# Kernel tuning notes

Hardware: AMD Instinct MI355X
Metric: run time of the kernel (lower is better)

Reference implementation:

```python
import jax, jax.numpy as jnp
import numpy as np

B_, S_, N_, D_ = 2, 128, 16, 6
HMV, HS, HEADS = 8, 24, 8

# ---- G(3,0,1) geometric algebra tables (16-dim multivectors) ----
_BLADES = [(), (0,), (1,), (2,), (3,), (0, 1), (0, 2), (0, 3), (1, 2), (1, 3), (2, 3), (0, 1, 2), (0, 1, 3), (0, 2, 3), (1, 2, 3), (0, 1, 2, 3)]
_IDX = {b: i for i, b in enumerate(_BLADES)}
_METRIC = [0.0, 1.0, 1.0, 1.0]  # e0^2=0 (projective), e1..e3^2=1

def _blade_mul(a, b):
    arr = list(a) + list(b)
    sign = 1.0
    i = 0
    while i < len(arr) - 1:
        if arr[i] > arr[i + 1]:
            arr[i], arr[i + 1] = arr[i + 1], arr[i]
            sign = -sign
            i = max(i - 1, 0)
        elif arr[i] == arr[i + 1]:
            sign *= _METRIC[arr[i]]
            del arr[i + 1]
            del arr[i]
            i = 0
        else:
            i += 1
    return sign, tuple(arr)

def _perm_sign(seq):
    s = 1.0
    for i in range(len(seq)):
        for j in range(i + 1, len(seq)):
            if seq[i] > seq[j]:
                s = -s
    return s

_GP_np = np.zeros((16, 16, 16), dtype=np.float32)
_WEDGE_np = np.zeros((16, 16, 16), dtype=np.float32)
for _a in _BLADES:
    for _b in _BLADES:
        _s, _r = _blade_mul(_a, _b)
        if _s != 0.0:
            _GP_np[_IDX[_r], _IDX[_a], _IDX[_b]] += _s
        if not set(_a) & set(_b):
            _WEDGE_np[_IDX[tuple(sorted(_a + _b))], _IDX[_a], _IDX[_b]] += _perm_sign(list(_a) + list(_b))

_DUAL_np = np.zeros((16, 16), dtype=np.float32)
for _b in _BLADES:
    _c = tuple(sorted(set((0, 1, 2, 3)) - set(_b)))
    _DUAL_np[_IDX[_c], _IDX[_b]] = _perm_sign(list(_b) + list(_c))

# 9 Pin-equivariant linear basis maps: 5 grade projections + 4 e0-wedge maps
_BASIS_np = np.zeros((9, 16, 16), dtype=np.float32)
for _i, _b in enumerate(_BLADES):
    _BASIS_np[len(_b), _i, _i] = 1.0
    if 0 not in _b and len(_b) <= 3:
        _BASIS_np[5 + len(_b), _IDX[(0,) + _b], _i] = 1.0

GP = jnp.asarray(_GP_np)
WEDGE = jnp.asarray(_WEDGE_np)
DUAL = jnp.asarray(_DUAL_np)
BASIS = jnp.asarray(_BASIS_np)
# invariant inner product uses the 8 non-e0 components
INNER = jnp.asarray(np.array([1, 0, 1, 1, 1, 0, 0, 0, 1, 1, 1, 0, 0, 0, 1, 0], dtype=np.float32))


def equi_linear(x_mv, x_s, w_mv, w_s2mv, w_m2s, w_s2s, b_mv, b_s):
    # x_mv [..., in_ch, 16] -> [..., out_ch, 16]; scalar channels mix via mv comp 0
    y = jnp.einsum('oik,kpq,...iq->...op', w_mv, BASIS, x_mv)
    extra = 0.0
    if w_s2mv is not None:
        extra = extra + jnp.einsum('oi,...i->...o', w_s2mv, x_s)
    if b_mv is not None:
        extra = extra + b_mv
    if w_s2mv is not None or b_mv is not None:
        y = y.at[..., 0].add(extra)
    y_s = None
    if w_m2s is not None:
        y_s = jnp.einsum('oi,...i->...o', w_m2s, x_mv[..., 0])
        if w_s2s is not None:
            y_s = y_s + jnp.einsum('oi,...i->...o', w_s2s, x_s)
        if b_s is not None:
            y_s = y_s + b_s
    return y, y_s


def equi_norm(x_mv, x_s, eps=1e-2):
    sq = jnp.sum(x_mv * x_mv * INNER, axis=-1)  # [..., ch]
    x_mv = x_mv / jnp.sqrt(jnp.mean(sq, axis=-1, keepdims=True) + eps)[..., None]
    x_s = x_s / jnp.sqrt(jnp.mean(x_s * x_s, axis=-1, keepdims=True) + eps)
    return x_mv, x_s


def join(a, b):
    da = jnp.einsum('pq,...q->...p', DUAL, a)
    db = jnp.einsum('pq,...q->...p', DUAL, b)
    w = jnp.einsum('kij,...i,...j->...k', WEDGE, da, db)
    return jnp.einsum('qp,...q->...p', DUAL, w)  # undual = DUAL^T (signed permutation)


def _forward(x, p):
    B, S, N, D = x.shape
    T = S * N
    xf = x.reshape(B, T, D)
    pos, vel = xf[..., 0:3], xf[..., 3:6]
    mv = jnp.zeros((B, T, 16), xf.dtype)
    mv = mv.at[..., 0].set(1.0)           # embed_scalar(mass=1)
    mv = mv.at[..., 14].set(1.0)          # embed_point: homogeneous e123
    mv = mv.at[..., 13].set(-pos[..., 0])
    mv = mv.at[..., 12].set(pos[..., 1])
    mv = mv.at[..., 11].set(-pos[..., 2])
    mv = mv.at[..., 5:8].set(0.5 * vel)   # embed_translation versor bivector part
    mv = mv[:, :, None, :]                # [B,T,1,16]

    times = jnp.arange(T) // N
    mask = times[:, None] >= times[None, :]  # causal over time blocks

    h_mv, h_s = equi_linear(mv, None, p['w_in_mv'], None, p['w_in_m2s'], None, p['b_in_mv'], p['b_in_s'])

    # --- equivariant self-attention block ---
    n_mv, n_s = equi_norm(h_mv, h_s)
    q_mv, q_s = equi_linear(n_mv, n_s, p['w_qkv_mv'][0], p['w_qkv_s2mv'][0], p['w_qkv_m2s'][0], p['w_qkv_s2s'][0], None, None)
    k_mv, k_s = equi_linear(n_mv, n_s, p['w_qkv_mv'][1], p['w_qkv_s2mv'][1], p['w_qkv_m2s'][1], p['w_qkv_s2s'][1], None, None)
    v_mv, v_s = equi_linear(n_mv, n_s, p['w_qkv_mv'][2], p['w_qkv_s2mv'][2], p['w_qkv_m2s'][2], p['w_qkv_s2s'][2], None, None)
    H = HEADS
    rs = lambda m, s: (m.reshape(B, T, H, HMV // H, 16), s.reshape(B, T, H, HS // H))
    q_mv, q_s = rs(q_mv, q_s)
    k_mv, k_s = rs(k_mv, k_s)
    v_mv, v_s = rs(v_mv, v_s)
    scale = 1.0 / np.sqrt(8.0 * (HMV // H) + HS // H)
    scores = (jnp.einsum('bthcq,q,bshcq->bhts', q_mv, INNER, k_mv)
              + jnp.einsum('bthd,bshd->bhts', q_s, k_s)) * scale
    scores = jnp.where(mask[None, None], scores, -1e30)
    attn = jax.nn.softmax(scores, axis=-1)
    o_mv = jnp.einsum('bhts,bshcq->bthcq', attn, v_mv).reshape(B, T, HMV, 16)
    o_s = jnp.einsum('bhts,bshd->bthd', attn, v_s).reshape(B, T, HS)
    a_mv, a_s = equi_linear(o_mv, o_s, p['w_ao_mv'], p['w_ao_s2mv'], p['w_ao_m2s'], p['w_ao_s2s'], p['b_ao_mv'], p['b_ao_s'])
    h_mv = h_mv + a_mv
    h_s = h_s + a_s

    # --- geometric MLP block ---
    n_mv, n_s = equi_norm(h_mv, h_s)
    u_mv, u_s = equi_linear(n_mv, n_s, p['w_m1_mv'], p['w_m1_s2mv'], p['w_m1_m2s'], p['w_m1_s2s'], p['b_m1_mv'], p['b_m1_s'])
    gl, gr, jl, jr = jnp.split(u_mv, 4, axis=-2)  # 4 groups of HMV/2 channels
    gp = jnp.einsum('kij,btci,btcj->btck', GP, gl, gr)  # geometric product
    jn = join(jl, jr)                                   # dual-based join
    g_mv = jnp.concatenate([gp, jn], axis=-2)           # [B,T,HMV,16]
    g_mv = g_mv * jax.nn.gelu(g_mv[..., 0:1], approximate=False)  # scalar-gated GELU
    g_s = jax.nn.gelu(u_s, approximate=False)
    m_mv, m_s = equi_linear(g_mv, g_s, p['w_m2_mv'], p['w_m2_s2mv'], p['w_m2_m2s'], p['w_m2_s2s'], p['b_m2_mv'], p['b_m2_s'])
    h_mv = h_mv + m_mv
    h_s = h_s + m_s

    out_mv, _ = equi_linear(h_mv, h_s, p['w_out_mv'], p['w_out_s2mv'], None, None, p['b_out_mv'], None)
    o = out_mv[:, :, 0, :]
    d = o[..., 14:15]
    d = jnp.where(jnp.abs(d) > 1e-3, d, jnp.where(d >= 0, 1e-3, -1e-3))  # safe homogeneous divide
    pred_pos = jnp.stack([-o[..., 13], o[..., 12], -o[..., 11]], axis=-1) / d  # extract_point
    pred_vel = 2.0 * o[..., 5:8]                                              # extract_translation
    return jnp.concatenate([pred_pos, pred_vel], axis=-1).reshape(B, S, N, D)


def setup_inputs() -> dict:
    key = jax.random.key(0)
    ks = iter(jax.random.split(key, 40))
    def nrm(shape, fan):
        return jax.random.normal(next(ks), shape, jnp.float32) / np.sqrt(fan)
    inp = {}
    inp['x'] = jax.random.normal(next(ks), (B_, S_, N_, D_), jnp.float32)
    inp['w_in_mv'] = nrm((HMV, 1, 9), 3.0)
    inp['b_in_mv'] = jnp.zeros((HMV,), jnp.float32)
    inp['w_in_m2s'] = nrm((HS, 1), 1.0)
    inp['b_in_s'] = jnp.zeros((HS,), jnp.float32)
    inp['w_qkv_mv'] = nrm((3, HMV, HMV, 9), 3.0 * HMV)
    inp['w_qkv_s2mv'] = nrm((3, HMV, HS), HS)
    inp['w_qkv_m2s'] = nrm((3, HS, HMV), HMV)
    inp['w_qkv_s2s'] = nrm((3, HS, HS), HS)
    inp['w_ao_mv'] = nrm((HMV, HMV, 9), 3.0 * HMV)
    inp['w_ao_s2mv'] = nrm((HMV, HS), HS)
    inp['w_ao_m2s'] = nrm((HS, HMV), HMV)
    inp['w_ao_s2s'] = nrm((HS, HS), HS)
    inp['b_ao_mv'] = jnp.zeros((HMV,), jnp.float32)
    inp['b_ao_s'] = jnp.zeros((HS,), jnp.float32)
    inp['w_m1_mv'] = nrm((2 * HMV, HMV, 9), 3.0 * HMV)
    inp['w_m1_s2mv'] = nrm((2 * HMV, HS), HS)
    inp['w_m1_m2s'] = nrm((HS, HMV), HMV)
    inp['w_m1_s2s'] = nrm((HS, HS), HS)
    inp['b_m1_mv'] = jnp.zeros((2 * HMV,), jnp.float32)
    inp['b_m1_s'] = jnp.zeros((HS,), jnp.float32)
    inp['w_m2_mv'] = nrm((HMV, HMV, 9), 3.0 * HMV)
    inp['w_m2_s2mv'] = nrm((HMV, HS), HS)
    inp['w_m2_m2s'] = nrm((HS, HMV), HMV)
    inp['w_m2_s2s'] = nrm((HS, HS), HS)
    inp['b_m2_mv'] = jnp.zeros((HMV,), jnp.float32)
    inp['b_m2_s'] = jnp.zeros((HS,), jnp.float32)
    inp['w_out_mv'] = nrm((1, HMV, 9), 3.0 * HMV)
    inp['w_out_s2mv'] = nrm((1, HS), HS)
    inp['b_out_mv'] = jnp.zeros((1,), jnp.float32)
    return inp


def reference(x, w_in_mv, b_in_mv, w_in_m2s, b_in_s, w_qkv_mv, w_qkv_s2mv, w_qkv_m2s, w_qkv_s2s, w_ao_mv, w_ao_s2mv, w_ao_m2s, w_ao_s2s, b_ao_mv, b_ao_s, w_m1_mv, w_m1_s2mv, w_m1_m2s, w_m1_s2s, b_m1_mv, b_m1_s, w_m2_mv, w_m2_s2mv, w_m2_m2s, w_m2_s2s, b_m2_mv, b_m2_s, w_out_mv, w_out_s2mv, b_out_mv):
    p = dict(locals())
    xx = p.pop('x')
    return _forward(xx, p)
```

## Files before the change

### kernel.cpp

```cpp
#include <hip/hip_runtime.h>
#include <math.h>

#define T_    2048
#define BTOK  4096
#define NSLOT 80

namespace {
constexpr int GRADE[16] = {0,1,1,1,1,2,2,2,2,2,2,3,3,3,3,4};
constexpr int AUGK[16]  = {-1,5,-1,-1,-1,6,6,6,-1,-1,-1,7,7,7,-1,8};
constexpr int AUGS[16]  = { 0,0, 0, 0, 0,2,3,4, 0, 0, 0,8,9,10,0,14};
constexpr float FINNER[16] = {1.f,0.f,1.f,1.f,1.f,0.f,0.f,0.f,1.f,1.f,1.f,0.f,0.f,0.f,1.f,0.f};
}

typedef __attribute__((ext_vector_type(4))) _Float16 h4_t;
typedef __attribute__((ext_vector_type(4))) float    f4_t;

__device__ __forceinline__ unsigned pkh(float a, float b){
  return __builtin_bit_cast(unsigned, __builtin_amdgcn_cvt_pkrtz(a,b));
}
__device__ __forceinline__ f4_t mfma16(h4_t a, h4_t b, f4_t c){
  return __builtin_amdgcn_mfma_f32_16x16x16f16(a,b,c,0,0,0);
}

__device__ __forceinline__ float gelu_f(float v){
  return 0.5f*v*(1.f + erff(v*0.70710678118654752f));
}

__device__ __forceinline__ int rsign_d(int a, int b){
  int s=0; a>>=1; while(a){ s += __popc(a&b); a>>=1; } return (s&1) ? -1 : 1;
}

__global__ void __launch_bounds__(64) k_in(
    const float* __restrict__ x,
    const float* __restrict__ w_in_mv, const float* __restrict__ b_in_mv,
    const float* __restrict__ w_in_m2s, const float* __restrict__ b_in_s,
    const float* __restrict__ w_mv, const float* __restrict__ w_s2mv,
    const float* __restrict__ w_m2s, const float* __restrict__ w_s2s,
    float* __restrict__ h_mv, float* __restrict__ h_s,
    unsigned* __restrict__ qph, unsigned* __restrict__ kph, unsigned* __restrict__ vph)
{
  __shared__ float NS[2*152];
  int tid=threadIdx.x, tl=tid>>5, ln=tid&31;
  int o=ln&7, iq=ln>>3;
  int tt=blockIdx.x*2+tl;
  int b=tt>>11, t=tt&(T_-1);
  const float* xp = x+(size_t)tt*6;
  float mv[16];
  #pragma unroll
  for(int p=0;p<16;p++) mv[p]=0.f;
  mv[0]=1.f; mv[14]=1.f;
  mv[13]=-xp[0]; mv[12]=xp[1]; mv[11]=-xp[2];
  mv[5]=0.5f*xp[3]; mv[6]=0.5f*xp[4]; mv[7]=0.5f*xp[5];

  const float* wo=w_in_mv+o*9;
  float h[16]; float sq=0.f;
  #pragma unroll
  for(int p=0;p<16;p++){
    float v=wo[GRADE[p]]*mv[p];
    if(AUGK[p]>=0) v+=wo[AUGK[p]]*mv[AUGS[p]];
    if(p==0) v+=b_in_mv[o];
    h[p]=v; sq+=FINNER[p]*v*v;
  }
  sq+=__shfl_xor(sq,1); sq+=__shfl_xor(sq,2); sq+=__shfl_xor(sq,4);
  float dmv=rsqrtf(sq*0.125f+0.01f);
  float hs[3]; float ssq=0.f;
  #pragma unroll
  for(int jj=0;jj<3;jj++){ float v=w_in_m2s[o*3+jj]+b_in_s[o*3+jj]; hs[jj]=v; ssq+=v*v; }
  ssq+=__shfl_xor(ssq,1); ssq+=__shfl_xor(ssq,2); ssq+=__shfl_xor(ssq,4);
  float dss=rsqrtf(ssq*(1.f/24.f)+0.01f);

  float* ns=&NS[tl*152];
  if(iq==0){
    float4* hg=(float4*)(h_mv+(size_t)tt*128+o*16);
    hg[0]=make_float4(h[0],h[1],h[2],h[3]);
    hg[1]=make_float4(h[4],h[5],h[6],h[7]);
    hg[2]=make_float4(h[8],h[9],h[10],h[11]);
    hg[3]=make_float4(h[12],h[13],h[14],h[15]);
    #pragma unroll
    for(int jj=0;jj<3;jj++) h_s[(size_t)tt*24+o*3+jj]=hs[jj];
    #pragma unroll
    for(int p=0;p<16;p++) ns[o*16+p]=h[p]*dmv;
    #pragma unroll
    for(int jj=0;jj<3;jj++) ns[128+o*3+jj]=hs[jj]*dss;
  }
  __syncthreads();

  float yq[16],yk[16],yv[16];
  #pragma unroll
  for(int p=0;p<16;p++){ yq[p]=0.f; yk[p]=0.f; yv[p]=0.f; }
  float nx0p[2];
  const float* wq=w_mv+o*72;
  #pragma unroll
  for(int ii=0;ii<2;ii++){
    int i=iq*2+ii;
    float xi[16];
    const float4* xs4=(const float4*)&ns[i*16];
    #pragma unroll
    for(int r4=0;r4<4;r4++){ float4 v=xs4[r4]; xi[r4*4]=v.x; xi[r4*4+1]=v.y; xi[r4*4+2]=v.z; xi[r4*4+3]=v.w; }
    nx0p[ii]=xi[0];
    const float* aq=wq+i*9; const float* ak=aq+576; const float* av=aq+1152;
    #pragma unroll
    for(int p=0;p<16;p++){
      float bb=xi[p];
      yq[p]+=aq[GRADE[p]]*bb; yk[p]+=ak[GRADE[p]]*bb; yv[p]+=av[GRADE[p]]*bb;
      if(AUGK[p]>=0){
        float au=xi[AUGS[p]];
        yq[p]+=aq[AUGK[p]]*au; yk[p]+=ak[AUGK[p]]*au; yv[p]+=av[AUGK[p]]*au;
      }
    }
  }
  float sq3[3]={0,0,0}, sk3[3]={0,0,0}, sv3[3]={0,0,0};
  float eq=0.f,ek=0.f,ev=0.f;
  for(int j=iq*6;j<iq*6+6;j++){
    float s=ns[128+j];
    eq+=w_s2mv[o*24+j]*s; ek+=w_s2mv[192+o*24+j]*s; ev+=w_s2mv[384+o*24+j]*s;
    #pragma unroll
    for(int jj=0;jj<3;jj++){
      int d=o*3+jj;
      sq3[jj]+=w_s2s[d*24+j]*s;
      sk3[jj]+=w_s2s[576+d*24+j]*s;
      sv3[jj]+=w_s2s[1152+d*24+j]*s;
    }
  }
  #pragma unroll
  for(int ii=0;ii<2;ii++){
    int i=iq*2+ii;
    #pragma unroll
    for(int jj=0;jj<3;jj++){
      int d=o*3+jj;
      sq3[jj]+=w_m2s[d*8+i]*nx0p[ii];
      sk3[jj]+=w_m2s[192+d*8+i]*nx0p[ii];
      sv3[jj]+=w_m2s[384+d*8+i]*nx0p[ii];
    }
  }
  yq[0]+=eq; yk[0]+=ek; yv[0]+=ev;
  #pragma unroll
  for(int p=0;p<16;p++){
    yq[p]+=__shfl_xor(yq[p],8);  yq[p]+=__shfl_xor(yq[p],16);
    yk[p]+=__shfl_xor(yk[p],8);  yk[p]+=__shfl_xor(yk[p],16);
    yv[p]+=__shfl_xor(yv[p],8);  yv[p]+=__shfl_xor(yv[p],16);
  }
  #pragma unroll
  for(int jj=0;jj<3;jj++){
    sq3[jj]+=__shfl_xor(sq3[jj],8); sq3[jj]+=__shfl_xor(sq3[jj],16);
    sk3[jj]+=__shfl_xor(sk3[jj],8); sk3[jj]+=__shfl_xor(sk3[jj],16);
    sv3[jj]+=__shfl_xor(sv3[jj],8); sv3[jj]+=__shfl_xor(sv3[jj],16);
  }

  const float scale = 0.3015113445777636f;
  size_t rb=((size_t)(b*8+o)*T_+t);
  if(iq==0){
    uint4 qa,qb;
    qa.x=pkh(yq[0]*scale, yq[2]*scale);  qa.y=pkh(yq[3]*scale, yq[4]*scale);
    qa.z=pkh(yq[8]*scale, yq[9]*scale);  qa.w=pkh(yq[10]*scale, yq[14]*scale);
    qb.x=pkh(sq3[0]*scale, sq3[1]*scale); qb.y=pkh(sq3[2]*scale, 0.f); qb.z=0u; qb.w=0u;
    uint4* qr4=(uint4*)qph + rb*2; qr4[0]=qa; qr4[1]=qb;
  } else if(iq==1){
    uint4 ka,kb;
    ka.x=pkh(yk[0],yk[2]);  ka.y=pkh(yk[3],yk[4]);
    ka.z=pkh(yk[8],yk[9]);  ka.w=pkh(yk[10],yk[14]);
    kb.x=pkh(sk3[0],sk3[1]); kb.y=pkh(sk3[2],0.f); kb.z=0u; kb.w=0u;
    uint4* kr4=(uint4*)kph + rb*2; kr4[0]=ka; kr4[1]=kb;
  }
  {
    size_t vbase2 = (size_t)(b*8+o)*(T_/16)*256;
    size_t cidx   = (size_t)(t>>4);
    int    wp     = (t>>1)&7;
    size_t tb     = vbase2 + cidx*256;
    bool even = (tl==0);
    if(iq==2){
      #pragma unroll
      for(int c=0;c<10;c++){
        float other=__shfl_xor(yv[c],32);
        if(even) vph[tb + c*8 + wp]=pkh(yv[c],other);
      }
    } else if(iq==3){
      #pragma unroll
      for(int c=10;c<16;c++){
        float other=__shfl_xor(yv[c],32);
        if(even) vph[tb + c*8 + wp]=pkh(yv[c],other);
      }
      #pragma unroll
      for(int jj=0;jj<3;jj++){
        float other=__shfl_xor(sv3[jj],32);
        if(even) vph[tb + (16+jj)*8 + wp]=pkh(sv3[jj],other);
      }
      if(even) vph[tb + 19*8 + wp]=0x3C003C00u;
    }
    if(even){
      int c0=20+iq*3;
      #pragma unroll
      for(int cc=0;cc<3;cc++) vph[tb + (c0+cc)*8 + wp]=0u;
    }
  }
}

__global__ void __launch_bounds__(256) k_attn(
    const unsigned* __restrict__ qph, const unsigned* __restrict__ kph,
    const unsigned* __restrict__ vph,
    float* __restrict__ part)
{
  int tid=threadIdx.x;
  int wave=tid>>6, lane=tid&63;
  int col=lane&15, rowb=lane>>4;
  int j=blockIdx.x;
  int bh=j&15;
  int z=NSLOT-1-(j>>4);
  int a=0;
  while (4*(a+1)*(a+2) <= z) a++;
  int rem = z - 4*a*(a+1);
  int bqd = rem/(a+1);
  int sp  = rem - bqd*(a+1);
  int strip = 8*a + bqd;
  int c     = a+1;
  int nchunk = (strip+1)*4;
  int t0 = sp*nchunk/c, t1 = (sp+1)*nchunk/c;
  int chend = strip*4 + wave + 1;
  if (t1 < chend) chend = t1;

  int q0 = strip*64 + wave*16;
  const h4_t* qh4=(const h4_t*)qph;
  const h4_t* kh4=(const h4_t*)kph;
  const h4_t* vh4=(const h4_t*)vph;

  h4_t bq = qh4[((size_t)bh*T_ + q0 + col)*4 + rowb];

  f4_t acc0={0.f,0.f,0.f,0.f}, acc1={0.f,0.f,0.f,0.f};
  size_t vtile = (size_t)bh*(T_/16)*128;
  int voff0 = col*4 + rowb;
  int voff1 = 64 + col*4 + rowb;

  #pragma unroll 4
  for(int ch=t0; ch<chend; ++ch){
    h4_t ak = kh4[((size_t)bh*T_ + 16*ch + col)*4 + rowb];
    f4_t zz={0.f,0.f,0.f,0.f};
    f4_t st = mfma16(ak, bq, zz);
    float c0=fminf(__expf(st[0]),60000.f);
    float c1=fminf(__expf(st[1]),60000.f);
    float c2=fminf(__expf(st[2]),60000.f);
    float c3=fminf(__expf(st[3]),60000.f);
    h4_t bp = __builtin_bit_cast(h4_t, make_uint2(pkh(c0,c1), pkh(c2,c3)));
    h4_t av0 = vh4[vtile + (size_t)ch*128 + voff0];
    h4_t av1 = vh4[vtile + (size_t)ch*128 + voff1];
    acc0 = mfma16(av0, bp, acc0);
    acc1 = mfma16(av1, bp, acc1);
  }

  float* rec = part + (((size_t)bh*NSLOT + z)*64 + wave*16 + col)*20;
  ((float4*)rec)[rowb] = make_float4(acc0[0],acc0[1],acc0[2],acc0[3]);
  if(rowb==0) ((float4*)rec)[4] = make_float4(acc1[0],acc1[1],acc1[2],acc1[3]);
}

__global__ void __launch_bounds__(64) k_tail(
    const float* __restrict__ part,
    const float* __restrict__ w_ao_mv, const float* __restrict__ w_ao_s2mv,
    const float* __restrict__ w_ao_m2s, const float* __restrict__ w_ao_s2s,
    const float* __restrict__ b_ao_mv, const float* __restrict__ b_ao_s,
    const float* __restrict__ h_mv, const float* __restrict__ h_s,
    const float* __restrict__ w_m1_mv, const float* __restrict__ w_m1_s2mv,
    const float* __restrict__ w_m1_m2s, const float* __restrict__ w_m1_s2s,
    const float* __restrict__ b_m1_mv, const float* __restrict__ b_m1_s,
    const float* __restrict__ w_m2_mv, const float* __restrict__ w_m2_s2mv,
    const float* __restrict__ b_m2_mv,
    const float* __restrict__ w_out_mv,
    float* __restrict__ out)
{
  __shared__ int   GPI[256]; __shared__ float GPS[256];
  __shared__ int   JNI[256]; __shared__ float JNS[256];
  __shared__ float OS[2*152];
  __shared__ float NS[2*152];
  __shared__ float U[2*264];
  __shared__ float G[2*136];
  __shared__ float GSm[2*24];
  int tid=threadIdx.x, tl=tid>>5, ln=tid&31;
  int o=ln&7, iq=ln>>3;
  int tt=blockIdx.x*2+tl;

  {
    const int mask_of[16]={0,1,2,4,8,3,5,9,6,10,12,7,11,13,14,15};
    const int idx_of[16] ={0,1,2,5,3,6,8,11,4,7,9,12,10,13,14,15};
    if (tid<16){
      int k=tid, km=mask_of[k], slotn=0;
      for(int i=0;i<16;i++){
        int im=mask_of[i], jm=im^km;
        if(im & jm & 1) continue;
        GPI[k*16+slotn]=i|(idx_of[jm]<<4);
        GPS[k*16+slotn]=(float)rsign_d(im,jm);
        slotn++;
      }
      for(;slotn<16;slotn++){ GPI[k*16+slotn]=0; GPS[k*16+slotn]=0.f; }
    } else if (tid<32){
      int p=tid-16, pm=mask_of[p], rest=15&~pm, slotn=0;
      for(int u=0;u<16;u++){
        if(u & ~rest) continue;
        int am=pm|u, bm=pm|(rest&~u);
        float s=(float)( rsign_d(pm,15&~pm)*rsign_d(15&~am,15&~bm)
                        *rsign_d(am,15&~am)*rsign_d(bm,15&~bm) );
        JNI[p*16+slotn]=idx_of[am]|(idx_of[bm]<<4);
        JNS[p*16+slotn]=s;
        slotn++;
      }
      for(;slotn<16;slotn++){ JNI[p*16+slotn]=0; JNS[p*16+slotn]=0.f; }
    }
  }

  {
    int b=tt>>11, t=tt&(T_-1);
    int strip=t>>6, qil=t&63;
    int h=ln>>2, qr=ln&3;
    int aa=strip>>3;
    int nsp=aa+1;
    int rbase=4*aa*(aa+1)+(strip&7)*(aa+1);
    const float* pb = part + ((size_t)((b*8+h)*NSLOT+rbase)*64 + qil)*20;
    float am[4]={0,0,0,0};
    float lv=0.f, s0=0.f, s1=0.f, s2=0.f;
    for(int spp=0; spp<nsp; ++spp){
      const float4* p4=(const float4*)(pb + (size_t)spp*64*20);
      float4 a4=p4[qr];
      am[0]+=a4.x; am[1]+=a4.y; am[2]+=a4.z; am[3]+=a4.w;
      if(qr==0){ float4 meta=p4[4]; s0+=meta.x; s1+=meta.y; s2+=meta.z; lv+=meta.w; }
    }
    float inv = (qr==0)? 1.f/lv : 0.f;
    inv = __shfl(inv, (tid & ~3));
    float* os=&OS[tl*152];
    #pragma unroll
    for(int p=0;p<4;p++) os[h*16+qr*4+p]=am[p]*inv;
    if(qr==0){ os[128+h*3]=s0*inv; os[128+h*3+1]=s1*inv; os[128+h*3+2]=s2*inv; }
  }
  __syncthreads();

  const float* os=&OS[tl*152];
  float xh[2][16];
  #pragma unroll
  for(int ii=0;ii<2;ii++){
    #pragma unroll
    for(int p=0;p<16;p++) xh[ii][p]=os[(iq*2+ii)*16+p];
  }
  float xs[24];
  #pragma unroll
  for(int jj=0;jj<24;jj++) xs[jj]=os[128+jj];

  float y[16];
  #pragma unroll
  for(int p=0;p<16;p++) y[p]=0.f;
  #pragma unroll
  for(int ii=0;ii<2;ii++){
    const float* wi=w_ao_mv+o*72+(iq*2+ii)*9;
    #pragma unroll
    for(int p=0;p<16;p++){
      y[p]+=wi[GRADE[p]]*xh[ii][p];
      if(AUGK[p]>=0) y[p]+=wi[AUGK[p]]*xh[ii][AUGS[p]];
    }
  }
  float e=(iq==0)? b_ao_mv[o] : 0.f;
  for(int j2=iq*6;j2<iq*6+6;j2++) e+=w_ao_s2mv[o*24+j2]*xs[j2];
  y[0]+=e;
  float a3[3];
  #pragma unroll
  for(int jj=0;jj<3;jj++) a3[jj]=(iq==0)? b_ao_s[o*3+jj] : 0.f;
  #pragma unroll
  for(int ii=0;ii<2;ii++){
    #pragma unroll
    for(int jj=0;jj<3;jj++) a3[jj]+=w_ao_m2s[(o*3+jj)*8+(iq*2+ii)]*xh[ii][0];
  }
  for(int j2=iq*6;j2<iq*6+6;j2++){
    #pragma unroll
    for(int jj=0;jj<3;jj++) a3[jj]+=w_ao_s2s[(o*3+jj)*24+j2]*xs[j2];
  }
  #pragma unroll
  for(int p=0;p<16;p++){ y[p]+=__shfl_xor(y[p],8); y[p]+=__shfl_xor(y[p],16); }
  #pragma unroll
  for(int jj=0;jj<3;jj++){ a3[jj]+=__shfl_xor(a3[jj],8); a3[jj]+=__shfl_xor(a3[jj],16); }

  float hch[16]; float sqv=0.f;
  { const float4* hg=(const float4*)(h_mv+(size_t)tt*128+o*16);
    #pragma unroll
    for(int r4=0;r4<4;r4++){ float4 v=hg[r4];
      hch[r4*4]=v.x+y[r4*4]; hch[r4*4+1]=v.y+y[r4*4+1];
      hch[r4*4+2]=v.z+y[r4*4+2]; hch[r4*4+3]=v.w+y[r4*4+3]; } }
  #pragma unroll
  for(int p=0;p<16;p++) sqv+=FINNER[p]*hch[p]*hch[p];
  sqv+=__shfl_xor(sqv,1); sqv+=__shfl_xor(sqv,2); sqv+=__shfl_xor(sqv,4);
  float dmv=rsqrtf(sqv*0.125f+0.01f);
  float hs3[3]; float ssq=0.f;
  #pragma unroll
  for(int jj=0;jj<3;jj++){
    float v=h_s[(size_t)tt*24+o*3+jj]+a3[jj];
    hs3[jj]=v; ssq+=v*v;
  }
  ssq+=__shfl_xor(ssq,1); ssq+=__shfl_xor(ssq,2); ssq+=__shfl_xor(ssq,4);
  float dss=rsqrtf(ssq*(1.f/24.f)+0.01f);

  float* nsbuf=&NS[tl*152];
  if(iq==0){
    #pragma unroll
    for(int p=0;p<16;p++) nsbuf[o*16+p]=hch[p]*dmv;
    #pragma unroll
    for(int jj=0;jj<3;jj++) nsbuf[128+o*3+jj]=hs3[jj]*dss;
  }
  __syncthreads();

  {
    int ln16=ln&15, mh=ln>>4;
    float u[16];
    #pragma unroll
    for(int p=0;p<16;p++) u[p]=0.f;
    for(int i=mh*4;i<mh*4+4;i++){
      float xi[16];
      const float4* xs4=(const float4*)&nsbuf[i*16];
      #pragma unroll
      for(int r4=0;r4<4;r4++){ float4 v=xs4[r4]; xi[r4*4]=v.x; xi[r4*4+1]=v.y; xi[r4*4+2]=v.z; xi[r4*4+3]=v.w; }
      const float* wi=w_m1_mv+ln16*72+i*9;
      #pragma unroll
      for(int p=0;p<16;p++){
        u[p]+=wi[GRADE[p]]*xi[p];
        if(AUGK[p]>=0) u[p]+=wi[AUGK[p]]*xi[AUGS[p]];
      }
    }
    float e1=(mh==0)? b_m1_mv[ln16] : 0.f;
    for(int j2=mh*12;j2<mh*12+12;j2++) e1+=w_m1_s2mv[ln16*24+j2]*nsbuf[128+j2];
    u[0]+=e1;
    #pragma unroll
    for(int p=0;p<16;p++) u[p]+=__shfl_xor(u[p],16);
    if(mh==0){
      float* uu=&U[tl*264];
      #pragma unroll
      for(int p=0;p<16;p++) uu[ln16*16+p]=u[p];
    }
  }
  if(ln<8){
    float s3[3];
    #pragma unroll
    for(int jj=0;jj<3;jj++) s3[jj]=b_m1_s[o*3+jj];
    for(int j2=0;j2<24;j2++){
      float s=nsbuf[128+j2];
      #pragma unroll
      for(int jj=0;jj<3;jj++) s3[jj]+=w_m1_s2s[(o*3+jj)*24+j2]*s;
    }
    for(int i=0;i<8;i++){
      float x0=nsbuf[i*16];
      #pragma unroll
      for(int jj=0;jj<3;jj++) s3[jj]+=w_m1_m2s[(o*3+jj)*8+i]*x0;
    }
    #pragma unroll
    for(int jj=0;jj<3;jj++) GSm[tl*24+o*3+jj]=gelu_f(s3[jj]);
  }
  __syncthreads();

  {
    const int*   TI=(o<4)? GPI : JNI;
    const float* TS=(o<4)? GPS : JNS;
    const float* uu=&U[tl*264];
    const float* lft=&uu[((o<4)? o : (4+o))*16];
    const float* rgt=&uu[((o<4)? (4+o) : (8+o))*16];
    float g[4];
    #pragma unroll
    for(int kk=0;kk<4;kk++){
      int k=iq*4+kk;
      float accv=0.f;
      #pragma unroll
      for(int e2=0;e2<16;e2++){
        int ij=TI[k*16+e2]; float sg=TS[k*16+e2];
        accv += sg * lft[ij&15] * rgt[ij>>4];
      }
      g[kk]=accv;
    }
    float g0 = __shfl(g[0], (tid & ~0x18));
    float gt = gelu_f(g0);
    float* gg=&G[tl*136];
    #pragma unroll
    for(int kk=0;kk<4;kk++) gg[o*16+iq*4+kk]=g[kk]*gt;
  }
  __syncthreads();

  float y2[16];
  #pragma unroll
  for(int p=0;p<16;p++) y2[p]=0.f;
  #pragma unroll
  for(int ii=0;ii<2;ii++){
    float xi[16];
    const float4* gi=(const float4*)&G[tl*136+(iq*2+ii)*16];
    #pragma unroll
    for(int r4=0;r4<4;r4++){ float4 v=gi[r4]; xi[r4*4]=v.x; xi[r4*4+1]=v.y; xi[r4*4+2]=v.z; xi[r4*4+3]=v.w; }
    const float* wi=w_m2_mv+o*72+(iq*2+ii)*9;
    #pragma unroll
    for(int p=0;p<16;p++){
      y2[p]+=wi[GRADE[p]]*xi[p];
      if(AUGK[p]>=0) y2[p]+=wi[AUGK[p]]*xi[AUGS[p]];
    }
  }
  float e2=(iq==0)? b_m2_mv[o] : 0.f;
  for(int j2=iq*6;j2<iq*6+6;j2++) e2+=w_m2_s2mv[o*24+j2]*GSm[tl*24+j2];
  y2[0]+=e2;
  #pragma unroll
  for(int p=0;p<16;p++){ y2[p]+=__shfl_xor(y2[p],8); y2[p]+=__shfl_xor(y2[p],16); }

  float hf[16];
  #pragma unroll
  for(int p=0;p<16;p++) hf[p]=hch[p]+y2[p];

  const float* wout=w_out_mv+o*9;
  float c5 =wout[2]*hf[5] +wout[6]*hf[2];
  float c6 =wout[2]*hf[6] +wout[6]*hf[3];
  float c7 =wout[2]*hf[7] +wout[6]*hf[4];
  float c11=wout[3]*hf[11]+wout[7]*hf[8];
  float c12=wout[3]*hf[12]+wout[7]*hf[9];
  float c13=wout[3]*hf[13]+wout[7]*hf[10];
  float c14=wout[3]*hf[14];
  #pragma unroll
  for(int mk=1; mk<8; mk<<=1){
    c5+=__shfl_xor(c5,mk); c6+=__shfl_xor(c6,mk); c7+=__shfl_xor(c7,mk);
    c11+=__shfl_xor(c11,mk); c12+=__shfl_xor(c12,mk);
    c13+=__shfl_xor(c13,mk); c14+=__shfl_xor(c14,mk);
  }
  if(ln==0){
    float dd=c14;
    dd=(fabsf(dd)>0.001f)? dd : (dd>=0.f? 0.001f : -0.001f);
    float* op=out+(size_t)tt*6;
    op[0]=-c13/dd; op[1]=c12/dd; op[2]=-c11/dd;
    op[3]=2.f*c5; op[4]=2.f*c6; op[5]=2.f*c7;
  }
}

extern "C" void kernel_launch(void* const* d_in, const int* in_sizes, int n_in,
                              void* d_out, int out_size, void* d_ws, size_t ws_size,
                              hipStream_t stream)
{
  (void)in_sizes; (void)n_in; (void)out_size; (void)ws_size;
  const float* x         =(const float*)d_in[0];
  const float* w_in_mv   =(const float*)d_in[1];
  const float* b_in_mv   =(const float*)d_in[2];
  const float* w_in_m2s  =(const float*)d_in[3];
  const float* b_in_s    =(const float*)d_in[4];
  const float* w_qkv_mv  =(const float*)d_in[5];
  const float* w_qkv_s2mv=(const float*)d_in[6];
  const float* w_qkv_m2s =(const float*)d_in[7];
  const float* w_qkv_s2s =(const float*)d_in[8];
  const float* w_ao_mv   =(const float*)d_in[9];
  const float* w_ao_s2mv =(const float*)d_in[10];
  const float* w_ao_m2s  =(const float*)d_in[11];
  const float* w_ao_s2s  =(const float*)d_in[12];
  const float* b_ao_mv   =(const float*)d_in[13];
  const float* b_ao_s    =(const float*)d_in[14];
  const float* w_m1_mv   =(const float*)d_in[15];
  const float* w_m1_s2mv =(const float*)d_in[16];
  const float* w_m1_m2s  =(const float*)d_in[17];
  const float* w_m1_s2s  =(const float*)d_in[18];
  const float* b_m1_mv   =(const float*)d_in[19];
  const float* b_m1_s    =(const float*)d_in[20];
  const float* w_m2_mv   =(const float*)d_in[21];
  const float* w_m2_s2mv =(const float*)d_in[22];
  const float* b_m2_mv   =(const float*)d_in[25];
  const float* w_out_mv  =(const float*)d_in[27];
  float* outp=(float*)d_out;

  float* ws=(float*)d_ws;
  size_t off=0;
  float* h_mv = ws+off; off+=(size_t)BTOK*128;
  float* h_s  = ws+off; off+=(size_t)BTOK*24;
  unsigned* qph = (unsigned*)(ws+off); off+=(size_t)16*T_*8;
  unsigned* kph = (unsigned*)(ws+off); off+=(size_t)16*T_*8;
  unsigned* vph = (unsigned*)(ws+off); off+=(size_t)16*(T_/16)*256;
  float* part = ws+off; off+=(size_t)16*NSLOT*64*20;

  k_in  <<<BTOK/2,64,0,stream>>>(x,w_in_mv,b_in_mv,w_in_m2s,b_in_s,
                                 w_qkv_mv,w_qkv_s2mv,w_qkv_m2s,w_qkv_s2s,
                                 h_mv,h_s,qph,kph,vph);
  k_attn<<<16*NSLOT,256,0,stream>>>(qph,kph,vph,part);
  k_tail<<<BTOK/2,64,0,stream>>>(part,
                                 w_ao_mv,w_ao_s2mv,w_ao_m2s,w_ao_s2s,b_ao_mv,b_ao_s,
                                 h_mv,h_s,
                                 w_m1_mv,w_m1_s2mv,w_m1_m2s,w_m1_s2s,b_m1_mv,b_m1_s,
                                 w_m2_mv,w_m2_s2mv,b_m2_mv,w_out_mv,outp);
}
```

Before: 58.39 us.

## Spread k_in and k_tail work over full wavefronts, one token per wave

k_in now uses one 64-lane wave per token (128 threads per block) instead of half a wave, so each lane handles one input channel. The V tile is packed through shared memory after a barrier instead of cross-lane shuffles. k_tail now runs one token per 64-thread block with twice as many blocks, and its partial-sum merge reads the normalizer from the fifth float4 slot. The aim is more parallelism and shorter per-lane serial chains, paid for with an extra shuffle stage and an extra barrier in k_in.

After: 65.66 us. 1.12x slower.

```diff
diff --git a/kernel.cpp b/kernel.cpp
--- a/kernel.cpp
+++ b/kernel.cpp
@@ -30,7 +30,7 @@
   int s=0; a>>=1; while(a){ s += __popc(a&b); a>>=1; } return (s&1) ? -1 : 1;
 }
 
-__global__ void __launch_bounds__(64) k_in(
+__global__ void __launch_bounds__(128) k_in(
     const float* __restrict__ x,
     const float* __restrict__ w_in_mv, const float* __restrict__ b_in_mv,
     const float* __restrict__ w_in_m2s, const float* __restrict__ b_in_s,
@@ -40,8 +40,9 @@
     unsigned* __restrict__ qph, unsigned* __restrict__ kph, unsigned* __restrict__ vph)
 {
   __shared__ float NS[2*152];
-  int tid=threadIdx.x, tl=tid>>5, ln=tid&31;
-  int o=ln&7, iq=ln>>3;
+  __shared__ float VX[2][8][19];
+  int tid=threadIdx.x, tl=tid>>6, ln=tid&63;
+  int o=ln&7, is=ln>>3;
   int tt=blockIdx.x*2+tl;
   int b=tt>>11, t=tt&(T_-1);
   const float* xp = x+(size_t)tt*6;
@@ -70,7 +71,7 @@
   float dss=rsqrtf(ssq*(1.f/24.f)+0.01f);
 
   float* ns=&NS[tl*152];
-  if(iq==0){
+  if(is==0){
     float4* hg=(float4*)(h_mv+(size_t)tt*128+o*16);
     hg[0]=make_float4(h[0],h[1],h[2],h[3]);
     hg[1]=make_float4(h[4],h[5],h[6],h[7]);
@@ -86,32 +87,27 @@
   __syncthreads();
 
   float yq[16],yk[16],yv[16];
-  #pragma unroll
-  for(int p=0;p<16;p++){ yq[p]=0.f; yk[p]=0.f; yv[p]=0.f; }
-  float nx0p[2];
-  const float* wq=w_mv+o*72;
-  #pragma unroll
-  for(int ii=0;ii<2;ii++){
-    int i=iq*2+ii;
-    float xi[16];
-    const float4* xs4=(const float4*)&ns[i*16];
-    #pragma unroll
-    for(int r4=0;r4<4;r4++){ float4 v=xs4[r4]; xi[r4*4]=v.x; xi[r4*4+1]=v.y; xi[r4*4+2]=v.z; xi[r4*4+3]=v.w; }
-    nx0p[ii]=xi[0];
-    const float* aq=wq+i*9; const float* ak=aq+576; const float* av=aq+1152;
-    #pragma unroll
-    for(int p=0;p<16;p++){
-      float bb=xi[p];
-      yq[p]+=aq[GRADE[p]]*bb; yk[p]+=ak[GRADE[p]]*bb; yv[p]+=av[GRADE[p]]*bb;
-      if(AUGK[p]>=0){
-        float au=xi[AUGS[p]];
-        yq[p]+=aq[AUGK[p]]*au; yk[p]+=ak[AUGK[p]]*au; yv[p]+=av[AUGK[p]]*au;
-      }
-    }
+  float xi[16];
+  { const float4* xs4=(const float4*)&ns[is*16];
+    #pragma unroll
+    for(int r4=0;r4<4;r4++){ float4 v=xs4[r4]; xi[r4*4]=v.x; xi[r4*4+1]=v.y; xi[r4*4+2]=v.z; xi[r4*4+3]=v.w; } }
+  float nx0=xi[0];
+  const float* aq=w_mv+o*72+is*9; const float* ak=aq+576; const float* av=aq+1152;
+  #pragma unroll
+  for(int p=0;p<16;p++){
+    float bb=xi[p];
+    float q_=aq[GRADE[p]]*bb, k_=ak[GRADE[p]]*bb, v_=av[GRADE[p]]*bb;
+    if(AUGK[p]>=0){
+      float au=xi[AUGS[p]];
+      q_+=aq[AUGK[p]]*au; k_+=ak[AUGK[p]]*au; v_+=av[AUGK[p]]*au;
+    }
+    yq[p]=q_; yk[p]=k_; yv[p]=v_;
   }
   float sq3[3]={0,0,0}, sk3[3]={0,0,0}, sv3[3]={0,0,0};
   float eq=0.f,ek=0.f,ev=0.f;
-  for(int j=iq*6;j<iq*6+6;j++){
+  #pragma unroll
+  for(int jo=0;jo<3;jo++){
+    int j=is*3+jo;
     float s=ns[128+j];
     eq+=w_s2mv[o*24+j]*s; ek+=w_s2mv[192+o*24+j]*s; ev+=w_s2mv[384+o*24+j]*s;
     #pragma unroll
@@ -123,74 +119,64 @@
     }
   }
   #pragma unroll
-  for(int ii=0;ii<2;ii++){
-    int i=iq*2+ii;
-    #pragma unroll
-    for(int jj=0;jj<3;jj++){
-      int d=o*3+jj;
-      sq3[jj]+=w_m2s[d*8+i]*nx0p[ii];
-      sk3[jj]+=w_m2s[192+d*8+i]*nx0p[ii];
-      sv3[jj]+=w_m2s[384+d*8+i]*nx0p[ii];
-    }
+  for(int jj=0;jj<3;jj++){
+    int d=o*3+jj;
+    sq3[jj]+=w_m2s[d*8+is]*nx0;
+    sk3[jj]+=w_m2s[192+d*8+is]*nx0;
+    sv3[jj]+=w_m2s[384+d*8+is]*nx0;
   }
   yq[0]+=eq; yk[0]+=ek; yv[0]+=ev;
   #pragma unroll
   for(int p=0;p<16;p++){
-    yq[p]+=__shfl_xor(yq[p],8);  yq[p]+=__shfl_xor(yq[p],16);
-    yk[p]+=__shfl_xor(yk[p],8);  yk[p]+=__shfl_xor(yk[p],16);
-    yv[p]+=__shfl_xor(yv[p],8);  yv[p]+=__shfl_xor(yv[p],16);
+    yq[p]+=__shfl_xor(yq[p],8);  yq[p]+=__shfl_xor(yq[p],16);  yq[p]+=__shfl_xor(yq[p],32);
+    yk[p]+=__shfl_xor(yk[p],8);  yk[p]+=__shfl_xor(yk[p],16);  yk[p]+=__shfl_xor(yk[p],32);
+    yv[p]+=__shfl_xor(yv[p],8);  yv[p]+=__shfl_xor(yv[p],16);  yv[p]+=__shfl_xor(yv[p],32);
   }
   #pragma unroll
   for(int jj=0;jj<3;jj++){
-    sq3[jj]+=__shfl_xor(sq3[jj],8); sq3[jj]+=__shfl_xor(sq3[jj],16);
-    sk3[jj]+=__shfl_xor(sk3[jj],8); sk3[jj]+=__shfl_xor(sk3[jj],16);
-    sv3[jj]+=__shfl_xor(sv3[jj],8); sv3[jj]+=__shfl_xor(sv3[jj],16);
+    sq3[jj]+=__shfl_xor(sq3[jj],8); sq3[jj]+=__shfl_xor(sq3[jj],16); sq3[jj]+=__shfl_xor(sq3[jj],32);
+    sk3[jj]+=__shfl_xor(sk3[jj],8); sk3[jj]+=__shfl_xor(sk3[jj],16); sk3[jj]+=__shfl_xor(sk3[jj],32);
+    sv3[jj]+=__shfl_xor(sv3[jj],8); sv3[jj]+=__shfl_xor(sv3[jj],16); sv3[jj]+=__shfl_xor(sv3[jj],32);
   }
 
   const float scale = 0.3015113445777636f;
   size_t rb=((size_t)(b*8+o)*T_+t);
-  if(iq==0){
+  if(is==0){
     uint4 qa,qb;
     qa.x=pkh(yq[0]*scale, yq[2]*scale);  qa.y=pkh(yq[3]*scale, yq[4]*scale);
     qa.z=pkh(yq[8]*scale, yq[9]*scale);  qa.w=pkh(yq[10]*scale, yq[14]*scale);
     qb.x=pkh(sq3[0]*scale, sq3[1]*scale); qb.y=pkh(sq3[2]*scale, 0.f); qb.z=0u; qb.w=0u;
     uint4* qr4=(uint4*)qph + rb*2; qr4[0]=qa; qr4[1]=qb;
-  } else if(iq==1){
+    #pragma unroll
+    for(int c=0;c<16;c++) VX[tl][o][c]=yv[c];
+    #pragma unroll
+    for(int jj=0;jj<3;jj++) VX[tl][o][16+jj]=sv3[jj];
+  } else if(is==1){
     uint4 ka,kb;
     ka.x=pkh(yk[0],yk[2]);  ka.y=pkh(yk[3],yk[4]);
     ka.z=pkh(yk[8],yk[9]);  ka.w=pkh(yk[10],yk[14]);
     kb.x=pkh(sk3[0],sk3[1]); kb.y=pkh(sk3[2],0.f); kb.z=0u; kb.w=0u;
     uint4* kr4=(uint4*)kph + rb*2; kr4[0]=ka; kr4[1]=kb;
   }
-  {
-    size_t vbase2 = (size_t)(b*8+o)*(T_/16)*256;
-    size_t cidx   = (size_t)(t>>4);
-    int    wp     = (t>>1)&7;
-    size_t tb     = vbase2 + cidx*256;
-    bool even = (tl==0);
-    if(iq==2){
-      #pragma unroll
-      for(int c=0;c<10;c++){
-        float other=__shfl_xor(yv[c],32);
-        if(even) vph[tb + c*8 + wp]=pkh(yv[c],other);
-      }
-    } else if(iq==3){
-      #pragma unroll
-      for(int c=10;c<16;c++){
-        float other=__shfl_xor(yv[c],32);
-        if(even) vph[tb + c*8 + wp]=pkh(yv[c],other);
-      }
-      #pragma unroll
-      for(int jj=0;jj<3;jj++){
-        float other=__shfl_xor(sv3[jj],32);
-        if(even) vph[tb + (16+jj)*8 + wp]=pkh(sv3[jj],other);
-      }
-      if(even) vph[tb + 19*8 + wp]=0x3C003C00u;
-    }
-    if(even){
-      int c0=20+iq*3;
-      #pragma unroll
-      for(int cc=0;cc<3;cc++) vph[tb + (c0+cc)*8 + wp]=0u;
+  __syncthreads();
+
+  if(tl==0){
+    int te=blockIdx.x*2 & (T_-1);
+    size_t tb = (size_t)(b*8+o)*(T_/16)*256 + (size_t)(te>>4)*256;
+    int wp = (te>>1)&7;
+    if(is==2){
+      #pragma unroll
+      for(int c=0;c<10;c++) vph[tb + c*8 + wp]=pkh(VX[0][o][c], VX[1][o][c]);
+    } else if(is==3){
+      #pragma unroll
+      for(int c=10;c<19;c++) vph[tb + c*8 + wp]=pkh(VX[0][o][c], VX[1][o][c]);
+      vph[tb + 19*8 + wp]=0x3C003C00u;
+    } else if(is==4){
+      #pragma unroll
+      for(int c=20;c<26;c++) vph[tb + c*8 + wp]=0u;
+    } else if(is==5){
+      #pragma unroll
+      for(int c=26;c<32;c++) vph[tb + c*8 + wp]=0u;
     }
   }
 }
@@ -267,14 +253,14 @@
 {
   __shared__ int   GPI[256]; __shared__ float GPS[256];
   __shared__ int   JNI[256]; __shared__ float JNS[256];
-  __shared__ float OS[2*152];
-  __shared__ float NS[2*152];
-  __shared__ float U[2*264];
-  __shared__ float G[2*136];
-  __shared__ float GSm[2*24];
-  int tid=threadIdx.x, tl=tid>>5, ln=tid&31;
-  int o=ln&7, iq=ln>>3;
-  int tt=blockIdx.x*2+tl;
+  __shared__ float OS[152];
+  __shared__ float NSb[152];
+  __shared__ float U[264];
+  __shared__ float G[136];
+  __shared__ float GSm[24];
+  int tid=threadIdx.x, ln=tid;
+  int o=ln&7, is=ln>>3;
+  int tt=blockIdx.x;
 
   {
     const int mask_of[16]={0,1,2,4,8,3,5,9,6,10,12,7,11,13,14,15};
@@ -307,70 +293,63 @@
   {
     int b=tt>>11, t=tt&(T_-1);
     int strip=t>>6, qil=t&63;
-    int h=ln>>2, qr=ln&3;
+    int h=ln>>3, fq=ln&7;
     int aa=strip>>3;
     int nsp=aa+1;
     int rbase=4*aa*(aa+1)+(strip&7)*(aa+1);
     const float* pb = part + ((size_t)((b*8+h)*NSLOT+rbase)*64 + qil)*20;
     float am[4]={0,0,0,0};
-    float lv=0.f, s0=0.f, s1=0.f, s2=0.f;
-    for(int spp=0; spp<nsp; ++spp){
-      const float4* p4=(const float4*)(pb + (size_t)spp*64*20);
-      float4 a4=p4[qr];
-      am[0]+=a4.x; am[1]+=a4.y; am[2]+=a4.z; am[3]+=a4.w;
-      if(qr==0){ float4 meta=p4[4]; s0+=meta.x; s1+=meta.y; s2+=meta.z; lv+=meta.w; }
-    }
-    float inv = (qr==0)? 1.f/lv : 0.f;
-    inv = __shfl(inv, (tid & ~3));
-    float* os=&OS[tl*152];
-    #pragma unroll
-    for(int p=0;p<4;p++) os[h*16+qr*4+p]=am[p]*inv;
-    if(qr==0){ os[128+h*3]=s0*inv; os[128+h*3+1]=s1*inv; os[128+h*3+2]=s2*inv; }
+    if(fq<5){
+      for(int spp=0; spp<nsp; ++spp){
+        const float4* p4=(const float4*)(pb + (size_t)spp*64*20);
+        float4 a4=p4[fq];
+        am[0]+=a4.x; am[1]+=a4.y; am[2]+=a4.z; am[3]+=a4.w;
+      }
+    }
+    float inv = 1.f/am[3];
+    inv = __shfl(inv, (ln & ~7) + 4);
+    if(fq<4){
+      #pragma unroll
+      for(int r=0;r<4;r++) OS[h*16+fq*4+r]=am[r]*inv;
+    } else if(fq==4){
+      OS[128+h*3+0]=am[0]*inv; OS[128+h*3+1]=am[1]*inv; OS[128+h*3+2]=am[2]*inv;
+    }
   }
   __syncthreads();
 
-  const float* os=&OS[tl*152];
-  float xh[2][16];
-  #pragma unroll
-  for(int ii=0;ii<2;ii++){
-    #pragma unroll
-    for(int p=0;p<16;p++) xh[ii][p]=os[(iq*2+ii)*16+p];
-  }
+  float xi[16];
+  { const float4* xs4=(const float4*)&OS[is*16];
+    #pragma unroll
+    for(int r4=0;r4<4;r4++){ float4 v=xs4[r4]; xi[r4*4]=v.x; xi[r4*4+1]=v.y; xi[r4*4+2]=v.z; xi[r4*4+3]=v.w; } }
   float xs[24];
   #pragma unroll
-  for(int jj=0;jj<24;jj++) xs[jj]=os[128+jj];
+  for(int jj=0;jj<24;jj++) xs[jj]=OS[128+jj];
 
   float y[16];
-  #pragma unroll
-  for(int p=0;p<16;p++) y[p]=0.f;
-  #pragma unroll
-  for(int ii=0;ii<2;ii++){
-    const float* wi=w_ao_mv+o*72+(iq*2+ii)*9;
+  { const float* wi=w_ao_mv+o*72+is*9;
     #pragma unroll
     for(int p=0;p<16;p++){
-      y[p]+=wi[GRADE[p]]*xh[ii][p];
-      if(AUGK[p]>=0) y[p]+=wi[AUGK[p]]*xh[ii][AUGS[p]];
-    }
-  }
-  float e=(iq==0)? b_ao_mv[o] : 0.f;
-  for(int j2=iq*6;j2<iq*6+6;j2++) e+=w_ao_s2mv[o*24+j2]*xs[j2];
+      float v=wi[GRADE[p]]*xi[p];
+      if(AUGK[p]>=0) v+=wi[AUGK[p]]*xi[AUGS[p]];
+      y[p]=v;
+    } }
+  float e=(is==0)? b_ao_mv[o] : 0.f;
+  #pragma unroll
+  for(int jo=0;jo<3;jo++) e+=w_ao_s2mv[o*24+is*3+jo]*xs[is*3+jo];
   y[0]+=e;
   float a3[3];
   #pragma unroll
-  for(int jj=0;jj<3;jj++) a3[jj]=(iq==0)? b_ao_s[o*3+jj] : 0.f;
-  #pragma unroll
-  for(int ii=0;ii<2;ii++){
-    #pragma unroll
-    for(int jj=0;jj<3;jj++) a3[jj]+=w_ao_m2s[(o*3+jj)*8+(iq*2+ii)]*xh[ii][0];
-  }
-  for(int j2=iq*6;j2<iq*6+6;j2++){
-    #pragma unroll
-    for(int jj=0;jj<3;jj++) a3[jj]+=w_ao_s2s[(o*3+jj)*24+j2]*xs[j2];
-  }
-  #pragma unroll
-  for(int p=0;p<16;p++){ y[p]+=__shfl_xor(y[p],8); y[p]+=__shfl_xor(y[p],16); }
-  #pragma unroll
-  for(int jj=0;jj<3;jj++){ a3[jj]+=__shfl_xor(a3[jj],8); a3[jj]+=__shfl_xor(a3[jj],16); }
+  for(int jj=0;jj<3;jj++){
+    float v=(is==0)? b_ao_s[o*3+jj] : 0.f;
+    v+=w_ao_m2s[(o*3+jj)*8+is]*xi[0];
+    #pragma unroll
+    for(int jo=0;jo<3;jo++) v+=w_ao_s2s[(o*3+jj)*24+is*3+jo]*xs[is*3+jo];
+    a3[jj]=v;
+  }
+  #pragma unroll
+  for(int p=0;p<16;p++){ y[p]+=__shfl_xor(y[p],8); y[p]+=__shfl_xor(y[p],16); y[p]+=__shfl_xor(y[p],32); }
+  #pragma unroll
+  for(int jj=0;jj<3;jj++){ a3[jj]+=__shfl_xor(a3[jj],8); a3[jj]+=__shfl_xor(a3[jj],16); a3[jj]+=__shfl_xor(a3[jj],32); }
 
   float hch[16]; float sqv=0.f;
   { const float4* hg=(const float4*)(h_mv+(size_t)tt*128+o*16);
@@ -391,12 +370,11 @@
   ssq+=__shfl_xor(ssq,1); ssq+=__shfl_xor(ssq,2); ssq+=__shfl_xor(ssq,4);
   float dss=rsqrtf(ssq*(1.f/24.f)+0.01f);
 
-  float* nsbuf=&NS[tl*152];
-  if(iq==0){
-    #pragma unroll
-    for(int p=0;p<16;p++) nsbuf[o*16+p]=hch[p]*dmv;
-    #pragma unroll
-    for(int jj=0;jj<3;jj++) nsbuf[128+o*3+jj]=hs3[jj]*dss;
+  if(is==0){
+    #pragma unroll
+    for(int p=0;p<16;p++) NSb[o*16+p]=hch[p]*dmv;
+    #pragma unroll
+    for(int jj=0;jj<3;jj++) NSb[128+o*3+jj]=hs3[jj]*dss;
   }
   __syncthreads();
 
@@ -405,58 +383,61 @@
     float u[16];
     #pragma unroll
     for(int p=0;p<16;p++) u[p]=0.f;
-    for(int i=mh*4;i<mh*4+4;i++){
-      float xi[16];
-      const float4* xs4=(const float4*)&nsbuf[i*16];
-      #pragma unroll
-      for(int r4=0;r4<4;r4++){ float4 v=xs4[r4]; xi[r4*4]=v.x; xi[r4*4+1]=v.y; xi[r4*4+2]=v.z; xi[r4*4+3]=v.w; }
+    #pragma unroll
+    for(int io=0;io<2;io++){
+      int i=mh*2+io;
+      float zi[16];
+      const float4* xs4=(const float4*)&NSb[i*16];
+      #pragma unroll
+      for(int r4=0;r4<4;r4++){ float4 v=xs4[r4]; zi[r4*4]=v.x; zi[r4*4+1]=v.y; zi[r4*4+2]=v.z; zi[r4*4+3]=v.w; }
       const float* wi=w_m1_mv+ln16*72+i*9;
       #pragma unroll
       for(int p=0;p<16;p++){
-        u[p]+=wi[GRADE[p]]*xi[p];
-        if(AUGK[p]>=0) u[p]+=wi[AUGK[p]]*xi[AUGS[p]];
+        u[p]+=wi[GRADE[p]]*zi[p];
+        if(AUGK[p]>=0) u[p]+=wi[AUGK[p]]*zi[AUGS[p]];
       }
     }
     float e1=(mh==0)? b_m1_mv[ln16] : 0.f;
-    for(int j2=mh*12;j2<mh*12+12;j2++) e1+=w_m1_s2mv[ln16*24+j2]*nsbuf[128+j2];
+    #pragma unroll
+    for(int jo=0;jo<6;jo++) e1+=w_m1_s2mv[ln16*24+mh*6+jo]*NSb[128+mh*6+jo];
     u[0]+=e1;
     #pragma unroll
-    for(int p=0;p<16;p++) u[p]+=__shfl_xor(u[p],16);
+    for(int p=0;p<16;p++){ u[p]+=__shfl_xor(u[p],16); u[p]+=__shfl_xor(u[p],32); }
     if(mh==0){
-      float* uu=&U[tl*264];
-      #pragma unroll
-      for(int p=0;p<16;p++) uu[ln16*16+p]=u[p];
-    }
-  }
-  if(ln<8){
-    float s3[3];
-    #pragma unroll
-    for(int jj=0;jj<3;jj++) s3[jj]=b_m1_s[o*3+jj];
-    for(int j2=0;j2<24;j2++){
-      float s=nsbuf[128+j2];
-      #pragma unroll
-      for(int jj=0;jj<3;jj++) s3[jj]+=w_m1_s2s[(o*3+jj)*24+j2]*s;
-    }
-    for(int i=0;i<8;i++){
-      float x0=nsbuf[i*16];
-      #pragma unroll
-      for(int jj=0;jj<3;jj++) s3[jj]+=w_m1_m2s[(o*3+jj)*8+i]*x0;
-    }
-    #pragma unroll
-    for(int jj=0;jj<3;jj++) GSm[tl*24+o*3+jj]=gelu_f(s3[jj]);
+      #pragma unroll
+      for(int p=0;p<16;p++) U[ln16*16+p]=u[p];
+    }
+  }
+  {
+    float s3[3]={0.f,0.f,0.f};
+    if(ln<16){
+      int o2=ln&7, hf2=ln>>3;
+      #pragma unroll
+      for(int jj=0;jj<3;jj++){
+        float v=(hf2==0)? b_m1_s[o2*3+jj] : 0.f;
+        for(int j2=hf2*12;j2<hf2*12+12;j2++) v+=w_m1_s2s[(o2*3+jj)*24+j2]*NSb[128+j2];
+        for(int i=hf2*4;i<hf2*4+4;i++)      v+=w_m1_m2s[(o2*3+jj)*8+i]*NSb[i*16];
+        s3[jj]=v;
+      }
+      #pragma unroll
+      for(int jj=0;jj<3;jj++) s3[jj]+=__shfl_xor(s3[jj],8);
+      if(hf2==0){
+        #pragma unroll
+        for(int jj=0;jj<3;jj++) GSm[o2*3+jj]=gelu_f(s3[jj]);
+      }
+    }
   }
   __syncthreads();
 
   {
     const int*   TI=(o<4)? GPI : JNI;
     const float* TS=(o<4)? GPS : JNS;
-    const float* uu=&U[tl*264];
-    const float* lft=&uu[((o<4)? o : (4+o))*16];
-    const float* rgt=&uu[((o<4)? (4+o) : (8+o))*16];
-    float g[4];
-    #pragma unroll
-    for(int kk=0;kk<4;kk++){
-      int k=iq*4+kk;
+    const float* lft=&U[((o<4)? o : (4+o))*16];
+    const float* rgt=&U[((o<4)? (4+o) : (8+o))*16];
+    float g[2];
+    #pragma unroll
+    for(int kk=0;kk<2;kk++){
+      int k=is*2+kk;
       float accv=0.f;
       #pragma unroll
       for(int e2=0;e2<16;e2++){
@@ -465,35 +446,31 @@
       }
       g[kk]=accv;
     }
-    float g0 = __shfl(g[0], (tid & ~0x18));
+    float g0 = __shfl(g[0], o);
     float gt = gelu_f(g0);
-    float* gg=&G[tl*136];
-    #pragma unroll
-    for(int kk=0;kk<4;kk++) gg[o*16+iq*4+kk]=g[kk]*gt;
+    G[o*16+is*2  ]=g[0]*gt;
+    G[o*16+is*2+1]=g[1]*gt;
   }
   __syncthreads();
 
   float y2[16];
-  #pragma unroll
-  for(int p=0;p<16;p++) y2[p]=0.f;
-  #pragma unroll
-  for(int ii=0;ii<2;ii++){
-    float xi[16];
-    const float4* gi=(const float4*)&G[tl*136+(iq*2+ii)*16];
-    #pragma unroll
-    for(int r4=0;r4<4;r4++){ float4 v=gi[r4]; xi[r4*4]=v.x; xi[r4*4+1]=v.y; xi[r4*4+2]=v.z; xi[r4*4+3]=v.w; }
-    const float* wi=w_m2_mv+o*72+(iq*2+ii)*9;
+  { float zi[16];
+    const float4* gi=(const float4*)&G[is*16];
+    #pragma unroll
+    for(int r4=0;r4<4;r4++){ float4 v=gi[r4]; zi[r4*4]=v.x; zi[r4*4+1]=v.y; zi[r4*4+2]=v.z; zi[r4*4+3]=v.w; }
+    const float* wi=w_m2_mv+o*72+is*9;
     #pragma unroll
     for(int p=0;p<16;p++){
-      y2[p]+=wi[GRADE[p]]*xi[p];
-      if(AUGK[p]>=0) y2[p]+=wi[AUGK[p]]*xi[AUGS[p]];
-    }
-  }
-  float e2=(iq==0)? b_m2_mv[o] : 0.f;
-  for(int j2=iq*6;j2<iq*6+6;j2++) e2+=w_m2_s2mv[o*24+j2]*GSm[tl*24+j2];
+      float v=wi[GRADE[p]]*zi[p];
+      if(AUGK[p]>=0) v+=wi[AUGK[p]]*zi[AUGS[p]];
+      y2[p]=v;
+    } }
+  float e2=(is==0)? b_m2_mv[o] : 0.f;
+  #pragma unroll
+  for(int jo=0;jo<3;jo++) e2+=w_m2_s2mv[o*24+is*3+jo]*GSm[is*3+jo];
   y2[0]+=e2;
   #pragma unroll
-  for(int p=0;p<16;p++){ y2[p]+=__shfl_xor(y2[p],8); y2[p]+=__shfl_xor(y2[p],16); }
+  for(int p=0;p<16;p++){ y2[p]+=__shfl_xor(y2[p],8); y2[p]+=__shfl_xor(y2[p],16); y2[p]+=__shfl_xor(y2[p],32); }
 
   float hf[16];
   #pragma unroll
@@ -563,13 +540,13 @@
   unsigned* vph = (unsigned*)(ws+off); off+=(size_t)16*(T_/16)*256;
   float* part = ws+off; off+=(size_t)16*NSLOT*64*20;
 
-  k_in  <<<BTOK/2,64,0,stream>>>(x,w_in_mv,b_in_mv,w_in_m2s,b_in_s,
-                                 w_qkv_mv,w_qkv_s2mv,w_qkv_m2s,w_qkv_s2s,
-                                 h_mv,h_s,qph,kph,vph);
+  k_in  <<<BTOK/2,128,0,stream>>>(x,w_in_mv,b_in_mv,w_in_m2s,b_in_s,
+                                  w_qkv_mv,w_qkv_s2mv,w_qkv_m2s,w_qkv_s2s,
+                                  h_mv,h_s,qph,kph,vph);
   k_attn<<<16*NSLOT,256,0,stream>>>(qph,kph,vph,part);
-  k_tail<<<BTOK/2,64,0,stream>>>(part,
-                                 w_ao_mv,w_ao_s2mv,w_ao_m2s,w_ao_s2s,b_ao_mv,b_ao_s,
-                                 h_mv,h_s,
-                                 w_m1_mv,w_m1_s2mv,w_m1_m2s,w_m1_s2s,b_m1_mv,b_m1_s,
-                                 w_m2_mv,w_m2_s2mv,b_m2_mv,w_out_mv,outp);
-}
+  k_tail<<<BTOK,64,0,stream>>>(part,
+                               w_ao_mv,w_ao_s2mv,w_ao_m2s,w_ao_s2s,b_ao_mv,b_ao_s,
+                               h_mv,h_s,
+                               w_m1_mv,w_m1_s2mv,w_m1_m2s,w_m1_s2s,b_m1_mv,b_m1_s,
+                               w_m2_mv,w_m2_s2mv,b_m2_mv,w_out_mv,outp);
+}
```
